# Kernel tuning notes

Measured on AMD Instinct MI355X. Metric: run time of the kernel, lower is better.

Reference implementation:

```python
import jax, jax.numpy as jnp
from jax import lax
import numpy as np

N = 262144
D_IN = 32
D_HID = 128
N_HIDDEN = 8          # total hidden Linear+ReLU layers (first + 7 repeated)
D_OUT = 16
D_COND_IN = 16
D_COND_OUT = 3


def setup_inputs() -> dict:
    key = jax.random.key(0)
    ks = jax.random.split(key, 8)
    s = 0.05  # stand-in for kaiming-uniform scale; math shape-faithful
    x = jax.random.normal(ks[0], (N, D_IN), dtype=jnp.float32)
    cond = jax.random.normal(ks[1], (N, D_COND_IN), dtype=jnp.float32)
    W0 = jax.random.normal(ks[2], (D_HID, D_IN), dtype=jnp.float32) * s
    Wh = jax.random.normal(ks[3], (N_HIDDEN - 1, D_HID, D_HID), dtype=jnp.float32) * s
    Wout = jax.random.normal(ks[4], (D_OUT, D_HID), dtype=jnp.float32) * s
    Wc0 = jax.random.normal(ks[5], (D_HID, D_HID + D_COND_IN), dtype=jnp.float32) * s
    Wc1 = jax.random.normal(ks[6], (D_HID // 2, D_HID), dtype=jnp.float32) * s
    Wc2 = jax.random.normal(ks[7], (D_COND_OUT, D_HID // 2), dtype=jnp.float32) * s
    return {"x": x, "cond": cond, "W0": W0, "Wh": Wh, "Wout": Wout,
            "Wc0": Wc0, "Wc1": Wc1, "Wc2": Wc2}


def reference(x, cond, W0, Wh, Wout, Wc0, Wc1, Wc2):
    # backbone: Linear(no bias) -> ReLU, repeated
    h = jax.nn.relu(x @ W0.T)                       # [N, D_HID]

    def step(h, W):
        return jax.nn.relu(h @ W.T), None

    h, _ = lax.scan(step, h, Wh)                    # 7 more Linear+ReLU layers

    uncond_x = h @ Wout.T                           # [N, D_OUT], no activation

    # conditional sub-net: Linear (NO activation) -> Linear -> ReLU -> Linear
    z = jnp.concatenate([h, cond], axis=-1) @ Wc0.T  # [N, D_HID]
    z = jax.nn.relu(z @ Wc1.T)                       # [N, D_HID//2]
    cond_x = z @ Wc2.T                               # [N, D_COND_OUT]
    return (uncond_x, cond_x)
```

## Files before the change

### kernel.cpp

```cpp
#include <hip/hip_runtime.h>
#include <hip/hip_bf16.h>
#include <stdint.h>


typedef __attribute__((ext_vector_type(8)))  short short8;
typedef __attribute__((ext_vector_type(16))) float f32x16;
typedef __attribute__((ext_vector_type(4)))  float float4v;

#define NTOT 262144

#define OFF_W0    0
#define SZ_W0     16384
#define OFF_WH(i) (16384 + (i) * 32768)
#define SZ_WH     32768
#define OFF_WOUT  245760
#define SZ_WOUT   8192
#define OFF_WC0H  253952
#define SZ_WC0H   32768
#define OFF_WC1   286720
#define SZ_WC1    16384
#define OFF_WC2   303104
#define SZ_WC2    4096
#define WS_TOTAL  307200

__device__ __forceinline__ unsigned short f2bf(float v) {
  union { __hip_bfloat16 h; unsigned short u; } c;
  c.h = __float2bfloat16(v);
  return c.u;
}

__global__ __launch_bounds__(256) void convw(
    const float* __restrict__ W0, const float* __restrict__ Wh,
    const float* __restrict__ Wout, const float* __restrict__ Wc0,
    const float* __restrict__ Wc1, const float* __restrict__ Wc2,
    unsigned char* __restrict__ ws) {
  int cid = blockIdx.x * 256 + threadIdx.x;
  if (cid >= WS_TOTAL / 16) return;
  int b = cid * 16;
  const float* src; int base, rows, K, SS, SK;
  if (b < 16384)       { base = 0;        src = W0;   rows = 128; SS = 32;  K = 32;  SK = 128; }
  else if (b < 245760) { int i = (b - 16384) >> 15;
                         base = 16384 + (i << 15);
                         src = Wh + i * 16384;        rows = 128; SS = 128; K = 128; SK = 256; }
  else if (b < 253952) { base = OFF_WOUT; src = Wout; rows = 16;  SS = 128; K = 128; SK = 256; }
  else if (b < 286720) { base = OFF_WC0H; src = Wc0;  rows = 128; SS = 144; K = 128; SK = 256; }
  else if (b < 303104) { base = OFF_WC1;  src = Wc1;  rows = 64;  SS = 128; K = 128; SK = 256; }
  else                 { base = OFF_WC2;  src = Wc2;  rows = 3;   SS = 64;  K = 64;  SK = 128; }
  int rel  = b - base;
  int row  = rel / SK;
  int o    = rel - row * SK;
  int M    = (SK >= 256) ? 15 : 7;
  int col0 = (o ^ ((row & M) << 4)) >> 1;
  unsigned w0 = 0, w1 = 0, w2 = 0, w3 = 0;
  if (row < rows && col0 < K) {
    const float* p = src + row * SS + col0;
    w0 = (unsigned)f2bf(p[0]) | ((unsigned)f2bf(p[1]) << 16);
    w1 = (unsigned)f2bf(p[2]) | ((unsigned)f2bf(p[3]) << 16);
    w2 = (unsigned)f2bf(p[4]) | ((unsigned)f2bf(p[5]) << 16);
    w3 = (unsigned)f2bf(p[6]) | ((unsigned)f2bf(p[7]) << 16);
  }
  *(uint4*)(ws + b) = make_uint4(w0, w1, w2, w3);
}

__device__ __forceinline__ unsigned pk2(float a, float b) {
  unsigned d;
  asm("v_cvt_pk_bf16_f32 %0, %1, %2" : "=v"(d) : "v"(a), "v"(b));
  return d;
}

__device__ __forceinline__ short8 frag_s8(const unsigned (&f)[4]) {
  union { unsigned u[4]; short8 s; } c;
  c.u[0] = f[0]; c.u[1] = f[1]; c.u[2] = f[2]; c.u[3] = f[3];
  return c.s;
}

__device__ __forceinline__ void swap32(unsigned &a, unsigned &b) {
  asm("v_permlane32_swap_b32 %0, %1" : "+v"(a), "+v"(b));
}

__device__ __forceinline__ void build2(const f32x16 &a,
                                       unsigned (&f0)[4], unsigned (&f1)[4]) {
  unsigned a00 = pk2(a[0], a[1]),   a01 = pk2(a[2], a[3]);
  unsigned b00 = pk2(a[4], a[5]),   b01 = pk2(a[6], a[7]);
  swap32(a00, b00); swap32(a01, b01);
  f0[0] = a00; f0[1] = a01; f0[2] = b00; f0[3] = b01;
  unsigned a10 = pk2(a[8],  a[9]),  a11 = pk2(a[10], a[11]);
  unsigned b10 = pk2(a[12], a[13]), b11 = pk2(a[14], a[15]);
  swap32(a10, b10); swap32(a11, b11);
  f1[0] = a10; f1[1] = a11; f1[2] = b10; f1[3] = b11;
}

__device__ __forceinline__ void stage(const unsigned char* __restrict__ g,
                                      unsigned char* l, int bytes,
                                      int wv, int lane) {
  #pragma unroll
  for (int base = wv * 1024; base < bytes; base += 4096) {
    __builtin_amdgcn_global_load_lds(
        (const __attribute__((address_space(1))) void*)(g + base + lane * 16),
        (__attribute__((address_space(3))) void*)(l + base), 16, 0, 0);
  }
}

#define WAITVM() asm volatile("s_waitcnt vmcnt(0)" ::: "memory")
#define SETPRIO(x) __builtin_amdgcn_s_setprio(x)
#define MFMA(A_, B_, C_) __builtin_amdgcn_mfma_f32_32x32x16_bf16(A_, B_, C_, 0, 0, 0)

template <int NKT, int SK, bool RELU>
__device__ __forceinline__ void layer4(const unsigned char* wlds,
                                       const unsigned (&cur)[2][8][4],
                                       unsigned (&nxt)[2][8][4],
                                       int n, int g, unsigned swz,
                                       const f32x16 &zero16) {
  #pragma unroll
  for (int tp = 0; tp < 2; ++tp) {
    f32x16 a[2][2];
    SETPRIO(1);
    #pragma unroll
    for (int kk = 0; kk < NKT; ++kk) {
      unsigned ko = ((unsigned)(kk * 32 + 16 * g)) ^ swz;
      short8 wf0 = *(const short8*)(wlds + (unsigned)((64 * tp + n) * SK) + ko);
      short8 wf1 = *(const short8*)(wlds + (unsigned)((64 * tp + 32 + n) * SK) + ko);
      if (kk == 0) {
        a[0][0] = MFMA(wf0, frag_s8(cur[0][0]), zero16);
        a[0][1] = MFMA(wf0, frag_s8(cur[1][0]), zero16);
        a[1][0] = MFMA(wf1, frag_s8(cur[0][0]), zero16);
        a[1][1] = MFMA(wf1, frag_s8(cur[1][0]), zero16);
      } else {
        a[0][0] = MFMA(wf0, frag_s8(cur[0][kk]), a[0][0]);
        a[0][1] = MFMA(wf0, frag_s8(cur[1][kk]), a[0][1]);
        a[1][0] = MFMA(wf1, frag_s8(cur[0][kk]), a[1][0]);
        a[1][1] = MFMA(wf1, frag_s8(cur[1][kk]), a[1][1]);
      }
    }
    SETPRIO(0);
    #pragma unroll
    for (int u = 0; u < 2; ++u)
      #pragma unroll
      for (int s = 0; s < 2; ++s) {
        if (RELU) {
          #pragma unroll
          for (int j = 0; j < 16; ++j) a[u][s][j] = fmaxf(a[u][s][j], 0.f);
        }
        build2(a[u][s], nxt[s][4 * tp + 2 * u], nxt[s][4 * tp + 2 * u + 1]);
      }
  }
}

__global__ __launch_bounds__(256, 2) void mlp_fused(
    const float* __restrict__ x, const float* __restrict__ cond,
    const float* __restrict__ wc0g, const unsigned char* __restrict__ ws,
    float* __restrict__ out) {
  __shared__ __align__(16) unsigned char lds[81920];
  unsigned char* const A = lds;
  unsigned char* const B = lds + 32768;
  unsigned char* const C = lds + 65536;

  const int tid  = threadIdx.x;
  const int lane = tid & 63;
  const int wv   = tid >> 6;
  const int g    = lane >> 5;
  const int n    = lane & 31;
  const int rowbase = blockIdx.x * 256 + wv * 64;
  const int r0 = rowbase + n;
  const int r1 = rowbase + 32 + n;
  const unsigned swz8  = (unsigned)((n & 7) << 4);
  const unsigned swz16 = (unsigned)((n & 15) << 4);

  f32x16 zero16;
  #pragma unroll
  for (int j = 0; j < 16; ++j) zero16[j] = 0.f;

  unsigned FA[2][8][4], FB[2][8][4];

  stage(ws + OFF_W0, A, SZ_W0, wv, lane);
  #pragma unroll
  for (int s = 0; s < 2; ++s) {
    int row = s ? r1 : r0;
    #pragma unroll
    for (int kk = 0; kk < 2; ++kk) {
      const float4v* p = (const float4v*)(x + row * 32 + kk * 16 + 8 * g);
      float4v u0 = p[0], u1 = p[1];
      FA[s][kk][0] = pk2(u0.x, u0.y);
      FA[s][kk][1] = pk2(u0.z, u0.w);
      FA[s][kk][2] = pk2(u1.x, u1.y);
      FA[s][kk][3] = pk2(u1.z, u1.w);
    }
  }
  WAITVM(); __syncthreads();

  stage(ws + OFF_WH(0), B, SZ_WH, wv, lane);
  layer4<2, 128, true>(A, FA, FB, n, g, swz8, zero16);
  WAITVM(); __syncthreads();

  stage(ws + OFF_WH(1), A, SZ_WH, wv, lane);
  layer4<8, 256, true>(B, FB, FA, n, g, swz16, zero16);
  WAITVM(); __syncthreads();

  stage(ws + OFF_WH(2), B, SZ_WH, wv, lane);
  layer4<8, 256, true>(A, FA, FB, n, g, swz16, zero16);
  WAITVM(); __syncthreads();

  stage(ws + OFF_WH(3), A, SZ_WH, wv, lane);
  layer4<8, 256, true>(B, FB, FA, n, g, swz16, zero16);
  WAITVM(); __syncthreads();

  stage(ws + OFF_WH(4), B, SZ_WH, wv, lane);
  layer4<8, 256, true>(A, FA, FB, n, g, swz16, zero16);
  WAITVM(); __syncthreads();

  stage(ws + OFF_WH(5), A, SZ_WH, wv, lane);
  layer4<8, 256, true>(B, FB, FA, n, g, swz16, zero16);
  WAITVM(); __syncthreads();

  stage(ws + OFF_WH(6), B, SZ_WH, wv, lane);
  layer4<8, 256, true>(A, FA, FB, n, g, swz16, zero16);
  WAITVM(); __syncthreads();

  stage(ws + OFF_WOUT, A, SZ_WOUT, wv, lane);
  layer4<8, 256, true>(B, FB, FA, n, g, swz16, zero16);
  WAITVM(); __syncthreads();

  stage(ws + OFF_WC0H, B, SZ_WC0H, wv, lane);
  stage(ws + OFF_WC1,  C, SZ_WC1,  wv, lane);
  unsigned CF[2][4];
  unsigned CW[4][4];
  {
    f32x16 a0, a1;
    SETPRIO(1);
    #pragma unroll
    for (int kk = 0; kk < 8; ++kk) {
      unsigned ko = ((unsigned)(kk * 32 + 16 * g)) ^ swz16;
      short8 wf = *(const short8*)(A + (unsigned)(n * 256) + ko);
      if (kk == 0) {
        a0 = MFMA(wf, frag_s8(FA[0][0]), zero16);
        a1 = MFMA(wf, frag_s8(FA[1][0]), zero16);
      } else {
        a0 = MFMA(wf, frag_s8(FA[0][kk]), a0);
        a1 = MFMA(wf, frag_s8(FA[1][kk]), a1);
      }
    }
    SETPRIO(0);
    *(float4v*)(out + r0 * 16 + 4 * g)     = (float4v){a0[0], a0[1], a0[2], a0[3]};
    *(float4v*)(out + r0 * 16 + 8 + 4 * g) = (float4v){a0[4], a0[5], a0[6], a0[7]};
    *(float4v*)(out + r1 * 16 + 4 * g)     = (float4v){a1[0], a1[1], a1[2], a1[3]};
    *(float4v*)(out + r1 * 16 + 8 + 4 * g) = (float4v){a1[4], a1[5], a1[6], a1[7]};
    #pragma unroll
    for (int s = 0; s < 2; ++s) {
      const float4v* q = (const float4v*)(cond + (s ? r1 : r0) * 16 + 8 * g);
      float4v c0 = q[0], c1 = q[1];
      CF[s][0] = pk2(c0.x, c0.y); CF[s][1] = pk2(c0.z, c0.w);
      CF[s][2] = pk2(c1.x, c1.y); CF[s][3] = pk2(c1.z, c1.w);
    }
    #pragma unroll
    for (int t = 0; t < 4; ++t) {
      const float4v* pc = (const float4v*)(wc0g + (32 * t + n) * 144 + 128 + 8 * g);
      float4v q0 = pc[0], q1 = pc[1];
      CW[t][0] = pk2(q0.x, q0.y); CW[t][1] = pk2(q0.z, q0.w);
      CW[t][2] = pk2(q1.x, q1.y); CW[t][3] = pk2(q1.z, q1.w);
    }
  }
  WAITVM(); __syncthreads();

  unsigned char* const zw = A + wv * 8192;
  f32x16 w2[2][2];

  #pragma unroll
  for (int th = 0; th < 2; ++th) {
    f32x16 z[2][2];
    SETPRIO(1);
    #pragma unroll
    for (int kk = 0; kk < 8; ++kk) {
      unsigned ko = ((unsigned)(kk * 32 + 16 * g)) ^ swz16;
      short8 wf0 = *(const short8*)(B + (unsigned)((64 * th + n) * 256) + ko);
      short8 wf1 = *(const short8*)(B + (unsigned)((64 * th + 32 + n) * 256) + ko);
      if (kk == 0) {
        z[0][0] = MFMA(wf0, frag_s8(FA[0][0]), zero16);
        z[0][1] = MFMA(wf0, frag_s8(FA[1][0]), zero16);
        z[1][0] = MFMA(wf1, frag_s8(FA[0][0]), zero16);
        z[1][1] = MFMA(wf1, frag_s8(FA[1][0]), zero16);
      } else {
        z[0][0] = MFMA(wf0, frag_s8(FA[0][kk]), z[0][0]);
        z[0][1] = MFMA(wf0, frag_s8(FA[1][kk]), z[0][1]);
        z[1][0] = MFMA(wf1, frag_s8(FA[0][kk]), z[1][0]);
        z[1][1] = MFMA(wf1, frag_s8(FA[1][kk]), z[1][1]);
      }
    }
    #pragma unroll
    for (int u = 0; u < 2; ++u) {
      z[u][0] = MFMA(frag_s8(CW[2 * th + u]), frag_s8(CF[0]), z[u][0]);
      z[u][1] = MFMA(frag_s8(CW[2 * th + u]), frag_s8(CF[1]), z[u][1]);
    }
    SETPRIO(0);
    #pragma unroll
    for (int u = 0; u < 2; ++u)
      #pragma unroll
      for (int q = 0; q < 4; ++q) {
        unsigned bo = ((unsigned)(64 * u + 16 * q + 8 * g)) ^ swz8;
        *(uint2*)(zw + n * 128 + bo) =
            make_uint2(pk2(z[u][0][4 * q], z[u][0][4 * q + 1]),
                       pk2(z[u][0][4 * q + 2], z[u][0][4 * q + 3]));
        *(uint2*)(zw + (32 + n) * 128 + bo) =
            make_uint2(pk2(z[u][1][4 * q], z[u][1][4 * q + 1]),
                       pk2(z[u][1][4 * q + 2], z[u][1][4 * q + 3]));
      }

    if (th == 1) {
      __syncthreads();
      stage(ws + OFF_WC2, B, SZ_WC2, wv, lane);
    }
    SETPRIO(1);
    #pragma unroll
    for (int kk = 0; kk < 4; ++kk) {
      unsigned koz = ((unsigned)(kk * 32 + 16 * g)) ^ swz8;
      unsigned kow = ((unsigned)((4 * th + kk) * 32 + 16 * g)) ^ swz16;
      short8 zf0 = *(const short8*)(zw + n * 128 + koz);
      short8 zf1 = *(const short8*)(zw + (32 + n) * 128 + koz);
      short8 wm0 = *(const short8*)(C + (unsigned)(n * 256) + kow);
      short8 wm1 = *(const short8*)(C + (unsigned)((32 + n) * 256) + kow);
      if (th == 0 && kk == 0) {
        w2[0][0] = MFMA(wm0, zf0, zero16);
        w2[0][1] = MFMA(wm0, zf1, zero16);
        w2[1][0] = MFMA(wm1, zf0, zero16);
        w2[1][1] = MFMA(wm1, zf1, zero16);
      } else {
        w2[0][0] = MFMA(wm0, zf0, w2[0][0]);
        w2[0][1] = MFMA(wm0, zf1, w2[0][1]);
        w2[1][0] = MFMA(wm1, zf0, w2[1][0]);
        w2[1][1] = MFMA(wm1, zf1, w2[1][1]);
      }
    }
    SETPRIO(0);
  }

  #pragma unroll
  for (int m = 0; m < 2; ++m)
    #pragma unroll
    for (int q = 0; q < 4; ++q) {
      unsigned bo = ((unsigned)(64 * m + 16 * q + 8 * g)) ^ swz8;
      *(uint2*)(zw + n * 128 + bo) =
          make_uint2(pk2(fmaxf(w2[m][0][4 * q], 0.f),     fmaxf(w2[m][0][4 * q + 1], 0.f)),
                     pk2(fmaxf(w2[m][0][4 * q + 2], 0.f), fmaxf(w2[m][0][4 * q + 3], 0.f)));
      *(uint2*)(zw + (32 + n) * 128 + bo) =
          make_uint2(pk2(fmaxf(w2[m][1][4 * q], 0.f),     fmaxf(w2[m][1][4 * q + 1], 0.f)),
                     pk2(fmaxf(w2[m][1][4 * q + 2], 0.f), fmaxf(w2[m][1][4 * q + 3], 0.f)));
    }
  WAITVM(); __syncthreads();

  {
    f32x16 a0, a1;
    #pragma unroll
    for (int kk = 0; kk < 4; ++kk) {
      unsigned ko = ((unsigned)(kk * 32 + 16 * g)) ^ swz8;
      short8 wf  = *(const short8*)(B + (unsigned)(n * 128) + ko);
      short8 zf0 = *(const short8*)(zw + n * 128 + ko);
      short8 zf1 = *(const short8*)(zw + (32 + n) * 128 + ko);
      if (kk == 0) {
        a0 = MFMA(wf, zf0, zero16);
        a1 = MFMA(wf, zf1, zero16);
      } else {
        a0 = MFMA(wf, zf0, a0);
        a1 = MFMA(wf, zf1, a1);
      }
    }
    float* outc = out + (size_t)NTOT * 16;
    if (g == 0) {
      outc[r0 * 3 + 0] = a0[0];
      outc[r0 * 3 + 1] = a0[1];
      outc[r0 * 3 + 2] = a0[2];
      outc[r1 * 3 + 0] = a1[0];
      outc[r1 * 3 + 1] = a1[1];
      outc[r1 * 3 + 2] = a1[2];
    }
  }
}

extern "C" void kernel_launch(void* const* d_in, const int* in_sizes, int n_in,
                              void* d_out, int out_size, void* d_ws, size_t ws_size,
                              hipStream_t stream) {
  const float* x    = (const float*)d_in[0];
  const float* cond = (const float*)d_in[1];
  const float* W0   = (const float*)d_in[2];
  const float* Wh   = (const float*)d_in[3];
  const float* Wout = (const float*)d_in[4];
  const float* Wc0  = (const float*)d_in[5];
  const float* Wc1  = (const float*)d_in[6];
  const float* Wc2  = (const float*)d_in[7];
  unsigned char* ws = (unsigned char*)d_ws;

  convw<<<dim3((WS_TOTAL / 16 + 255) / 256), dim3(256), 0, stream>>>(
      W0, Wh, Wout, Wc0, Wc1, Wc2, ws);
  mlp_fused<<<dim3(NTOT / 256), dim3(256), 0, stream>>>(
      x, cond, Wc0, ws, (float*)d_out);
}
```

Baseline: 81.94 us.

## Pre-swizzle weights into MFMA fragment order and triple-buffer half-layer LDS staging

The weight conversion kernel now writes weights in per-lane MFMA fragment order, so each lane reads its fragment from a contiguous LDS address with no XOR swizzle. The main kernel splits every layer into two half-phases and rotates three 16 KB LDS buffers, using partial vmcnt waits and raw s_barrier so the next half's weight loads overlap the current half's MFMAs. LDS use drops from 80 KB to 48 KB. The conditional branch is rebuilt so the intermediate z activations stay in registers instead of spilling to LDS. In exchange the vmcnt counts are hand-tuned and easy to get wrong, and bank conflicts may change with the new layout.

```diff
diff --git a/kernel.cpp b/kernel.cpp
--- a/kernel.cpp
+++ b/kernel.cpp
@@ -9,19 +9,13 @@
 
 #define NTOT 262144
 
-#define OFF_W0    0
-#define SZ_W0     16384
-#define OFF_WH(i) (16384 + (i) * 32768)
-#define SZ_WH     32768
-#define OFF_WOUT  245760
-#define SZ_WOUT   8192
-#define OFF_WC0H  253952
-#define SZ_WC0H   32768
-#define OFF_WC1   286720
-#define SZ_WC1    16384
-#define OFF_WC2   303104
-#define SZ_WC2    4096
-#define WS_TOTAL  307200
+#define CW0    0
+#define CWH(i) (8192 + (i) * 32768)
+#define CWOUT  237568
+#define CWC0   245760
+#define CWC1   278528
+#define CWC2   294912
+#define WS_TOTAL 299008
 
 __device__ __forceinline__ unsigned short f2bf(float v) {
   union { __hip_bfloat16 h; unsigned short u; } c;
@@ -37,23 +31,24 @@
   int cid = blockIdx.x * 256 + threadIdx.x;
   if (cid >= WS_TOTAL / 16) return;
   int b = cid * 16;
-  const float* src; int base, rows, K, SS, SK;
-  if (b < 16384)       { base = 0;        src = W0;   rows = 128; SS = 32;  K = 32;  SK = 128; }
-  else if (b < 245760) { int i = (b - 16384) >> 15;
-                         base = 16384 + (i << 15);
-                         src = Wh + i * 16384;        rows = 128; SS = 128; K = 128; SK = 256; }
-  else if (b < 253952) { base = OFF_WOUT; src = Wout; rows = 16;  SS = 128; K = 128; SK = 256; }
-  else if (b < 286720) { base = OFF_WC0H; src = Wc0;  rows = 128; SS = 144; K = 128; SK = 256; }
-  else if (b < 303104) { base = OFF_WC1;  src = Wc1;  rows = 64;  SS = 128; K = 128; SK = 256; }
-  else                 { base = OFF_WC2;  src = Wc2;  rows = 3;   SS = 64;  K = 64;  SK = 128; }
-  int rel  = b - base;
-  int row  = rel / SK;
-  int o    = rel - row * SK;
-  int M    = (SK >= 256) ? 15 : 7;
-  int col0 = (o ^ ((row & M) << 4)) >> 1;
+  const float* src; int base, rows, SS, NKT;
+  if (b < 8192)        { base = CW0;   src = W0;   rows = 128; SS = 32;  NKT = 2; }
+  else if (b < 237568) { int i = (b - 8192) >> 15;
+                         base = 8192 + (i << 15);
+                         src = Wh + i * 16384;      rows = 128; SS = 128; NKT = 8; }
+  else if (b < 245760) { base = CWOUT; src = Wout; rows = 16;  SS = 128; NKT = 8; }
+  else if (b < 278528) { base = CWC0;  src = Wc0;  rows = 128; SS = 144; NKT = 8; }
+  else if (b < 294912) { base = CWC1;  src = Wc1;  rows = 64;  SS = 128; NKT = 8; }
+  else                 { base = CWC2;  src = Wc2;  rows = 3;   SS = 64;  NKT = 4; }
+  int rel = b - base;
+  int c   = rel >> 10;
+  int t   = c / NKT, kk = c - t * NKT;
+  int l   = (rel & 1023) >> 4;
+  int n   = l & 31, g = l >> 5;
+  int row = 32 * t + n, col = 16 * kk + 8 * g;
   unsigned w0 = 0, w1 = 0, w2 = 0, w3 = 0;
-  if (row < rows && col0 < K) {
-    const float* p = src + row * SS + col0;
+  if (row < rows) {
+    const float* p = src + row * SS + col;
     w0 = (unsigned)f2bf(p[0]) | ((unsigned)f2bf(p[1]) << 16);
     w1 = (unsigned)f2bf(p[2]) | ((unsigned)f2bf(p[3]) << 16);
     w2 = (unsigned)f2bf(p[4]) | ((unsigned)f2bf(p[5]) << 16);
@@ -101,59 +96,90 @@
   }
 }
 
-#define WAITVM() asm volatile("s_waitcnt vmcnt(0)" ::: "memory")
+#define VMCNT_(N) asm volatile("s_waitcnt vmcnt(" #N ")" ::: "memory")
+#define VMCNT(N) VMCNT_(N)
+#define BAR() __builtin_amdgcn_s_barrier()
 #define SETPRIO(x) __builtin_amdgcn_s_setprio(x)
 #define MFMA(A_, B_, C_) __builtin_amdgcn_mfma_f32_32x32x16_bf16(A_, B_, C_, 0, 0, 0)
 
-template <int NKT, int SK, bool RELU>
-__device__ __forceinline__ void layer4(const unsigned char* wlds,
-                                       const unsigned (&cur)[2][8][4],
-                                       unsigned (&nxt)[2][8][4],
-                                       int n, int g, unsigned swz,
-                                       const f32x16 &zero16) {
-  #pragma unroll
-  for (int tp = 0; tp < 2; ++tp) {
-    f32x16 a[2][2];
-    SETPRIO(1);
-    #pragma unroll
-    for (int kk = 0; kk < NKT; ++kk) {
-      unsigned ko = ((unsigned)(kk * 32 + 16 * g)) ^ swz;
-      short8 wf0 = *(const short8*)(wlds + (unsigned)((64 * tp + n) * SK) + ko);
-      short8 wf1 = *(const short8*)(wlds + (unsigned)((64 * tp + 32 + n) * SK) + ko);
-      if (kk == 0) {
-        a[0][0] = MFMA(wf0, frag_s8(cur[0][0]), zero16);
-        a[0][1] = MFMA(wf0, frag_s8(cur[1][0]), zero16);
-        a[1][0] = MFMA(wf1, frag_s8(cur[0][0]), zero16);
-        a[1][1] = MFMA(wf1, frag_s8(cur[1][0]), zero16);
-      } else {
-        a[0][0] = MFMA(wf0, frag_s8(cur[0][kk]), a[0][0]);
-        a[0][1] = MFMA(wf0, frag_s8(cur[1][kk]), a[0][1]);
-        a[1][0] = MFMA(wf1, frag_s8(cur[0][kk]), a[1][0]);
-        a[1][1] = MFMA(wf1, frag_s8(cur[1][kk]), a[1][1]);
+template <int NKT, bool RELU>
+__device__ __forceinline__ void half_phase(const unsigned char* lb,
+                                           const unsigned (&cur)[2][8][4],
+                                           unsigned (&nxt)[2][8][4], int hb,
+                                           const f32x16 &zero16) {
+  f32x16 a[2][2];
+  SETPRIO(1);
+  #pragma unroll
+  for (int kk = 0; kk < NKT; ++kk) {
+    short8 wf0 = *(const short8*)(lb + kk * 1024);
+    short8 wf1 = *(const short8*)(lb + NKT * 1024 + kk * 1024);
+    if (kk == 0) {
+      a[0][0] = MFMA(wf0, frag_s8(cur[0][0]), zero16);
+      a[0][1] = MFMA(wf0, frag_s8(cur[1][0]), zero16);
+      a[1][0] = MFMA(wf1, frag_s8(cur[0][0]), zero16);
+      a[1][1] = MFMA(wf1, frag_s8(cur[1][0]), zero16);
+    } else {
+      a[0][0] = MFMA(wf0, frag_s8(cur[0][kk]), a[0][0]);
+      a[0][1] = MFMA(wf0, frag_s8(cur[1][kk]), a[0][1]);
+      a[1][0] = MFMA(wf1, frag_s8(cur[0][kk]), a[1][0]);
+      a[1][1] = MFMA(wf1, frag_s8(cur[1][kk]), a[1][1]);
+    }
+  }
+  SETPRIO(0);
+  #pragma unroll
+  for (int u = 0; u < 2; ++u)
+    #pragma unroll
+    for (int s = 0; s < 2; ++s) {
+      if (RELU) {
+        #pragma unroll
+        for (int j = 0; j < 16; ++j) a[u][s][j] = fmaxf(a[u][s][j], 0.f);
       }
-    }
-    SETPRIO(0);
-    #pragma unroll
-    for (int u = 0; u < 2; ++u)
-      #pragma unroll
-      for (int s = 0; s < 2; ++s) {
-        if (RELU) {
-          #pragma unroll
-          for (int j = 0; j < 16; ++j) a[u][s][j] = fmaxf(a[u][s][j], 0.f);
-        }
-        build2(a[u][s], nxt[s][4 * tp + 2 * u], nxt[s][4 * tp + 2 * u + 1]);
-      }
-  }
+      build2(a[u][s], nxt[s][hb + 2 * u], nxt[s][hb + 2 * u + 1]);
+    }
+}
+
+__device__ __forceinline__ void half_c9(const unsigned char* lb,
+                                        const unsigned (&cur)[2][8][4],
+                                        unsigned (&nxt)[2][8][4], int hb,
+                                        const unsigned (&cw0)[4],
+                                        const unsigned (&cw1)[4],
+                                        const unsigned (&cf)[2][4],
+                                        const f32x16 &zero16) {
+  f32x16 a[2][2];
+  SETPRIO(1);
+  #pragma unroll
+  for (int kk = 0; kk < 8; ++kk) {
+    short8 wf0 = *(const short8*)(lb + kk * 1024);
+    short8 wf1 = *(const short8*)(lb + 8192 + kk * 1024);
+    if (kk == 0) {
+      a[0][0] = MFMA(wf0, frag_s8(cur[0][0]), zero16);
+      a[0][1] = MFMA(wf0, frag_s8(cur[1][0]), zero16);
+      a[1][0] = MFMA(wf1, frag_s8(cur[0][0]), zero16);
+      a[1][1] = MFMA(wf1, frag_s8(cur[1][0]), zero16);
+    } else {
+      a[0][0] = MFMA(wf0, frag_s8(cur[0][kk]), a[0][0]);
+      a[0][1] = MFMA(wf0, frag_s8(cur[1][kk]), a[0][1]);
+      a[1][0] = MFMA(wf1, frag_s8(cur[0][kk]), a[1][0]);
+      a[1][1] = MFMA(wf1, frag_s8(cur[1][kk]), a[1][1]);
+    }
+  }
+  a[0][0] = MFMA(frag_s8(cw0), frag_s8(cf[0]), a[0][0]);
+  a[0][1] = MFMA(frag_s8(cw0), frag_s8(cf[1]), a[0][1]);
+  a[1][0] = MFMA(frag_s8(cw1), frag_s8(cf[0]), a[1][0]);
+  a[1][1] = MFMA(frag_s8(cw1), frag_s8(cf[1]), a[1][1]);
+  SETPRIO(0);
+  #pragma unroll
+  for (int u = 0; u < 2; ++u)
+    #pragma unroll
+    for (int s = 0; s < 2; ++s)
+      build2(a[u][s], nxt[s][hb + 2 * u], nxt[s][hb + 2 * u + 1]);
 }
 
 __global__ __launch_bounds__(256, 2) void mlp_fused(
     const float* __restrict__ x, const float* __restrict__ cond,
     const float* __restrict__ wc0g, const unsigned char* __restrict__ ws,
     float* __restrict__ out) {
-  __shared__ __align__(16) unsigned char lds[81920];
-  unsigned char* const A = lds;
-  unsigned char* const B = lds + 32768;
-  unsigned char* const C = lds + 65536;
+  __shared__ __align__(16) unsigned char lds[49152];
 
   const int tid  = threadIdx.x;
   const int lane = tid & 63;
@@ -163,8 +189,7 @@
   const int rowbase = blockIdx.x * 256 + wv * 64;
   const int r0 = rowbase + n;
   const int r1 = rowbase + 32 + n;
-  const unsigned swz8  = (unsigned)((n & 7) << 4);
-  const unsigned swz16 = (unsigned)((n & 15) << 4);
+  const unsigned char* ldsL = lds + lane * 16;
 
   f32x16 zero16;
   #pragma unroll
@@ -172,7 +197,6 @@
 
   unsigned FA[2][8][4], FB[2][8][4];
 
-  stage(ws + OFF_W0, A, SZ_W0, wv, lane);
   #pragma unroll
   for (int s = 0; s < 2; ++s) {
     int row = s ? r1 : r0;
@@ -186,51 +210,82 @@
       FA[s][kk][3] = pk2(u1.z, u1.w);
     }
   }
-  WAITVM(); __syncthreads();
-
-  stage(ws + OFF_WH(0), B, SZ_WH, wv, lane);
-  layer4<2, 128, true>(A, FA, FB, n, g, swz8, zero16);
-  WAITVM(); __syncthreads();
-
-  stage(ws + OFF_WH(1), A, SZ_WH, wv, lane);
-  layer4<8, 256, true>(B, FB, FA, n, g, swz16, zero16);
-  WAITVM(); __syncthreads();
-
-  stage(ws + OFF_WH(2), B, SZ_WH, wv, lane);
-  layer4<8, 256, true>(A, FA, FB, n, g, swz16, zero16);
-  WAITVM(); __syncthreads();
-
-  stage(ws + OFF_WH(3), A, SZ_WH, wv, lane);
-  layer4<8, 256, true>(B, FB, FA, n, g, swz16, zero16);
-  WAITVM(); __syncthreads();
-
-  stage(ws + OFF_WH(4), B, SZ_WH, wv, lane);
-  layer4<8, 256, true>(A, FA, FB, n, g, swz16, zero16);
-  WAITVM(); __syncthreads();
-
-  stage(ws + OFF_WH(5), A, SZ_WH, wv, lane);
-  layer4<8, 256, true>(B, FB, FA, n, g, swz16, zero16);
-  WAITVM(); __syncthreads();
-
-  stage(ws + OFF_WH(6), B, SZ_WH, wv, lane);
-  layer4<8, 256, true>(A, FA, FB, n, g, swz16, zero16);
-  WAITVM(); __syncthreads();
-
-  stage(ws + OFF_WOUT, A, SZ_WOUT, wv, lane);
-  layer4<8, 256, true>(B, FB, FA, n, g, swz16, zero16);
-  WAITVM(); __syncthreads();
-
-  stage(ws + OFF_WC0H, B, SZ_WC0H, wv, lane);
-  stage(ws + OFF_WC1,  C, SZ_WC1,  wv, lane);
+  stage(ws + CW0,        lds,         4096, wv, lane);
+  stage(ws + CW0 + 4096, lds + 16384, 4096, wv, lane);
+  VMCNT(1); BAR();
+
+  stage(ws + CWH(0),         lds + 32768, 16384, wv, lane);
+  half_phase<2, true>(ldsL,          FA, FB, 0, zero16);
+  VMCNT(4); BAR();
+  stage(ws + CWH(0) + 16384, lds,         16384, wv, lane);
+  half_phase<2, true>(ldsL + 16384,  FA, FB, 4, zero16);
+  VMCNT(4); BAR();
+
+  stage(ws + CWH(1),         lds + 16384, 16384, wv, lane);
+  half_phase<8, true>(ldsL + 32768,  FB, FA, 0, zero16);
+  VMCNT(4); BAR();
+  stage(ws + CWH(1) + 16384, lds + 32768, 16384, wv, lane);
+  half_phase<8, true>(ldsL,          FB, FA, 4, zero16);
+  VMCNT(4); BAR();
+
+  stage(ws + CWH(2),         lds,         16384, wv, lane);
+  half_phase<8, true>(ldsL + 16384,  FA, FB, 0, zero16);
+  VMCNT(4); BAR();
+  stage(ws + CWH(2) + 16384, lds + 16384, 16384, wv, lane);
+  half_phase<8, true>(ldsL + 32768,  FA, FB, 4, zero16);
+  VMCNT(4); BAR();
+
+  stage(ws + CWH(3),         lds + 32768, 16384, wv, lane);
+  half_phase<8, true>(ldsL,          FB, FA, 0, zero16);
+  VMCNT(4); BAR();
+  stage(ws + CWH(3) + 16384, lds,         16384, wv, lane);
+  half_phase<8, true>(ldsL + 16384,  FB, FA, 4, zero16);
+  VMCNT(4); BAR();
+
+  stage(ws + CWH(4),         lds + 16384, 16384, wv, lane);
+  half_phase<8, true>(ldsL + 32768,  FA, FB, 0, zero16);
+  VMCNT(4); BAR();
+  stage(ws + CWH(4) + 16384, lds + 32768, 16384, wv, lane);
+  half_phase<8, true>(ldsL,          FA, FB, 4, zero16);
+  VMCNT(4); BAR();
+
+  stage(ws + CWH(5),         lds,         16384, wv, lane);
+  half_phase<8, true>(ldsL + 16384,  FB, FA, 0, zero16);
+  VMCNT(4); BAR();
+  stage(ws + CWH(5) + 16384, lds + 16384, 16384, wv, lane);
+  half_phase<8, true>(ldsL + 32768,  FB, FA, 4, zero16);
+  VMCNT(4); BAR();
+
+  stage(ws + CWH(6),         lds + 32768, 16384, wv, lane);
+  half_phase<8, true>(ldsL,          FA, FB, 0, zero16);
+  VMCNT(4); BAR();
+  stage(ws + CWH(6) + 16384, lds,         16384, wv, lane);
+  half_phase<8, true>(ldsL + 16384,  FA, FB, 4, zero16);
+  VMCNT(4); BAR();
+
+  stage(ws + CWOUT, lds + 16384, 8192, wv, lane);
+  half_phase<8, true>(ldsL + 32768,  FB, FA, 0, zero16);
+  VMCNT(2); BAR();
+  stage(ws + CWC0, lds + 32768, 16384, wv, lane);
+  half_phase<8, true>(ldsL,          FB, FA, 4, zero16);
+  VMCNT(4); BAR();
+
   unsigned CF[2][4];
-  unsigned CW[4][4];
   {
+    stage(ws + CWC0 + 16384, lds, 16384, wv, lane);
+    #pragma unroll
+    for (int s = 0; s < 2; ++s) {
+      const float4v* q = (const float4v*)(cond + (s ? r1 : r0) * 16 + 8 * g);
+      float4v c0 = q[0], c1 = q[1];
+      CF[s][0] = pk2(c0.x, c0.y); CF[s][1] = pk2(c0.z, c0.w);
+      CF[s][2] = pk2(c1.x, c1.y); CF[s][3] = pk2(c1.z, c1.w);
+    }
+    const unsigned char* lb = ldsL + 16384;
     f32x16 a0, a1;
     SETPRIO(1);
     #pragma unroll
     for (int kk = 0; kk < 8; ++kk) {
-      unsigned ko = ((unsigned)(kk * 32 + 16 * g)) ^ swz16;
-      short8 wf = *(const short8*)(A + (unsigned)(n * 256) + ko);
+      short8 wf = *(const short8*)(lb + kk * 1024);
       if (kk == 0) {
         a0 = MFMA(wf, frag_s8(FA[0][0]), zero16);
         a1 = MFMA(wf, frag_s8(FA[1][0]), zero16);
@@ -244,122 +299,54 @@
     *(float4v*)(out + r0 * 16 + 8 + 4 * g) = (float4v){a0[4], a0[5], a0[6], a0[7]};
     *(float4v*)(out + r1 * 16 + 4 * g)     = (float4v){a1[0], a1[1], a1[2], a1[3]};
     *(float4v*)(out + r1 * 16 + 8 + 4 * g) = (float4v){a1[4], a1[5], a1[6], a1[7]};
-    #pragma unroll
-    for (int s = 0; s < 2; ++s) {
-      const float4v* q = (const float4v*)(cond + (s ? r1 : r0) * 16 + 8 * g);
-      float4v c0 = q[0], c1 = q[1];
-      CF[s][0] = pk2(c0.x, c0.y); CF[s][1] = pk2(c0.z, c0.w);
-      CF[s][2] = pk2(c1.x, c1.y); CF[s][3] = pk2(c1.z, c1.w);
-    }
-    #pragma unroll
-    for (int t = 0; t < 4; ++t) {
-      const float4v* pc = (const float4v*)(wc0g + (32 * t + n) * 144 + 128 + 8 * g);
+  }
+  VMCNT(12); BAR();
+
+  {
+    unsigned CW0r[4], CW1r[4];
+    #pragma unroll
+    for (int u = 0; u < 2; ++u) {
+      const float4v* pc = (const float4v*)(wc0g + (32 * u + n) * 144 + 128 + 8 * g);
       float4v q0 = pc[0], q1 = pc[1];
-      CW[t][0] = pk2(q0.x, q0.y); CW[t][1] = pk2(q0.z, q0.w);
-      CW[t][2] = pk2(q1.x, q1.y); CW[t][3] = pk2(q1.z, q1.w);
-    }
-  }
-  WAITVM(); __syncthreads();
-
-  unsigned char* const zw = A + wv * 8192;
-  f32x16 w2[2][2];
-
-  #pragma unroll
-  for (int th = 0; th < 2; ++th) {
-    f32x16 z[2][2];
-    SETPRIO(1);
-    #pragma unroll
-    for (int kk = 0; kk < 8; ++kk) {
-      unsigned ko = ((unsigned)(kk * 32 + 16 * g)) ^ swz16;
-      short8 wf0 = *(const short8*)(B + (unsigned)((64 * th + n) * 256) + ko);
-      short8 wf1 = *(const short8*)(B + (unsigned)((64 * th + 32 + n) * 256) + ko);
+      unsigned* cw = u ? CW1r : CW0r;
+      cw[0] = pk2(q0.x, q0.y); cw[1] = pk2(q0.z, q0.w);
+      cw[2] = pk2(q1.x, q1.y); cw[3] = pk2(q1.z, q1.w);
+    }
+    stage(ws + CWC1, lds, 16384, wv, lane);
+    half_c9(ldsL + 32768, FA, FB, 0, CW0r, CW1r, CF, zero16);
+  }
+  VMCNT(16); BAR();
+
+  {
+    unsigned CW0r[4], CW1r[4];
+    #pragma unroll
+    for (int u = 0; u < 2; ++u) {
+      const float4v* pc = (const float4v*)(wc0g + (32 * (2 + u) + n) * 144 + 128 + 8 * g);
+      float4v q0 = pc[0], q1 = pc[1];
+      unsigned* cw = u ? CW1r : CW0r;
+      cw[0] = pk2(q0.x, q0.y); cw[1] = pk2(q0.z, q0.w);
+      cw[2] = pk2(q1.x, q1.y); cw[3] = pk2(q1.z, q1.w);
+    }
+    stage(ws + CWC2, lds + 16384, 4096, wv, lane);
+    half_c9(ldsL, FA, FB, 4, CW0r, CW1r, CF, zero16);
+  }
+  VMCNT(5); BAR();
+
+  half_phase<8, true>(ldsL, FB, FA, 0, zero16);
+  VMCNT(0); BAR();
+
+  {
+    const unsigned char* lb = ldsL + 16384;
+    f32x16 a0, a1;
+    #pragma unroll
+    for (int kk = 0; kk < 4; ++kk) {
+      short8 wf = *(const short8*)(lb + kk * 1024);
       if (kk == 0) {
-        z[0][0] = MFMA(wf0, frag_s8(FA[0][0]), zero16);
-        z[0][1] = MFMA(wf0, frag_s8(FA[1][0]), zero16);
-        z[1][0] = MFMA(wf1, frag_s8(FA[0][0]), zero16);
-        z[1][1] = MFMA(wf1, frag_s8(FA[1][0]), zero16);
+        a0 = MFMA(wf, frag_s8(FA[0][0]), zero16);
+        a1 = MFMA(wf, frag_s8(FA[1][0]), zero16);
       } else {
-        z[0][0] = MFMA(wf0, frag_s8(FA[0][kk]), z[0][0]);
-        z[0][1] = MFMA(wf0, frag_s8(FA[1][kk]), z[0][1]);
-        z[1][0] = MFMA(wf1, frag_s8(FA[0][kk]), z[1][0]);
-        z[1][1] = MFMA(wf1, frag_s8(FA[1][kk]), z[1][1]);
-      }
-    }
-    #pragma unroll
-    for (int u = 0; u < 2; ++u) {
-      z[u][0] = MFMA(frag_s8(CW[2 * th + u]), frag_s8(CF[0]), z[u][0]);
-      z[u][1] = MFMA(frag_s8(CW[2 * th + u]), frag_s8(CF[1]), z[u][1]);
-    }
-    SETPRIO(0);
-    #pragma unroll
-    for (int u = 0; u < 2; ++u)
-      #pragma unroll
-      for (int q = 0; q < 4; ++q) {
-        unsigned bo = ((unsigned)(64 * u + 16 * q + 8 * g)) ^ swz8;
-        *(uint2*)(zw + n * 128 + bo) =
-            make_uint2(pk2(z[u][0][4 * q], z[u][0][4 * q + 1]),
-                       pk2(z[u][0][4 * q + 2], z[u][0][4 * q + 3]));
-        *(uint2*)(zw + (32 + n) * 128 + bo) =
-            make_uint2(pk2(z[u][1][4 * q], z[u][1][4 * q + 1]),
-                       pk2(z[u][1][4 * q + 2], z[u][1][4 * q + 3]));
-      }
-
-    if (th == 1) {
-      __syncthreads();
-      stage(ws + OFF_WC2, B, SZ_WC2, wv, lane);
-    }
-    SETPRIO(1);
-    #pragma unroll
-    for (int kk = 0; kk < 4; ++kk) {
-      unsigned koz = ((unsigned)(kk * 32 + 16 * g)) ^ swz8;
-      unsigned kow = ((unsigned)((4 * th + kk) * 32 + 16 * g)) ^ swz16;
-      short8 zf0 = *(const short8*)(zw + n * 128 + koz);
-      short8 zf1 = *(const short8*)(zw + (32 + n) * 128 + koz);
-      short8 wm0 = *(const short8*)(C + (unsigned)(n * 256) + kow);
-      short8 wm1 = *(const short8*)(C + (unsigned)((32 + n) * 256) + kow);
-      if (th == 0 && kk == 0) {
-        w2[0][0] = MFMA(wm0, zf0, zero16);
-        w2[0][1] = MFMA(wm0, zf1, zero16);
-        w2[1][0] = MFMA(wm1, zf0, zero16);
-        w2[1][1] = MFMA(wm1, zf1, zero16);
-      } else {
-        w2[0][0] = MFMA(wm0, zf0, w2[0][0]);
-        w2[0][1] = MFMA(wm0, zf1, w2[0][1]);
-        w2[1][0] = MFMA(wm1, zf0, w2[1][0]);
-        w2[1][1] = MFMA(wm1, zf1, w2[1][1]);
-      }
-    }
-    SETPRIO(0);
-  }
-
-  #pragma unroll
-  for (int m = 0; m < 2; ++m)
-    #pragma unroll
-    for (int q = 0; q < 4; ++q) {
-      unsigned bo = ((unsigned)(64 * m + 16 * q + 8 * g)) ^ swz8;
-      *(uint2*)(zw + n * 128 + bo) =
-          make_uint2(pk2(fmaxf(w2[m][0][4 * q], 0.f),     fmaxf(w2[m][0][4 * q + 1], 0.f)),
-                     pk2(fmaxf(w2[m][0][4 * q + 2], 0.f), fmaxf(w2[m][0][4 * q + 3], 0.f)));
-      *(uint2*)(zw + (32 + n) * 128 + bo) =
-          make_uint2(pk2(fmaxf(w2[m][1][4 * q], 0.f),     fmaxf(w2[m][1][4 * q + 1], 0.f)),
-                     pk2(fmaxf(w2[m][1][4 * q + 2], 0.f), fmaxf(w2[m][1][4 * q + 3], 0.f)));
-    }
-  WAITVM(); __syncthreads();
-
-  {
-    f32x16 a0, a1;
-    #pragma unroll
-    for (int kk = 0; kk < 4; ++kk) {
-      unsigned ko = ((unsigned)(kk * 32 + 16 * g)) ^ swz8;
-      short8 wf  = *(const short8*)(B + (unsigned)(n * 128) + ko);
-      short8 zf0 = *(const short8*)(zw + n * 128 + ko);
-      short8 zf1 = *(const short8*)(zw + (32 + n) * 128 + ko);
-      if (kk == 0) {
-        a0 = MFMA(wf, zf0, zero16);
-        a1 = MFMA(wf, zf1, zero16);
-      } else {
-        a0 = MFMA(wf, zf0, a0);
-        a1 = MFMA(wf, zf1, a1);
+        a0 = MFMA(wf, frag_s8(FA[0][kk]), a0);
+        a1 = MFMA(wf, frag_s8(FA[1][kk]), a1);
       }
     }
     float* outc = out + (size_t)NTOT * 16;
```

Result: faster. 79.43 us (-3.1%).
